# Performance work log

Hardware: AMD Instinct MI355X
Metric: run time of the kernel (lower is better)

The kernel has to match this reference:

```python
import jax, jax.numpy as jnp
import numpy as np

N, E, G = 50000, 800000, 512
F_IN, ED, NUM_CLASSES = 128, 3, 10
H1, C1, C2 = 4, 32, 64


def _add_self_loops(src, dst, eattr, n):
    # PyG add_self_loops with fill_value='mean': loop attr = mean of incoming edge attrs
    cnt = jax.ops.segment_sum(jnp.ones_like(dst, dtype=eattr.dtype), dst, num_segments=n)
    loop = jax.ops.segment_sum(eattr, dst, num_segments=n) / jnp.maximum(cnt, 1.0)[:, None]
    ar = jnp.arange(n)
    return (jnp.concatenate([src, ar]), jnp.concatenate([dst, ar]),
            jnp.concatenate([eattr, loop], axis=0))


def _gatv2(x, src, dst, eattr, Wl, bl, Wr, br, We, att, bias, heads, out_ch, concat, n):
    xl = (x @ Wl.T + bl).reshape(n, heads, out_ch)   # source transform (lin_l)
    xr = (x @ Wr.T + br).reshape(n, heads, out_ch)   # target transform (lin_r)
    ee = (eattr @ We.T).reshape(-1, heads, out_ch)   # edge transform (lin_edge, no bias)
    m = jax.nn.leaky_relu(xl[src] + xr[dst] + ee, 0.2)  # [E', H, C]
    score = jnp.einsum('ehc,hc->eh', m, att)
    # segment softmax over incoming edges of each target node
    smax = jax.ops.segment_max(score, dst, num_segments=n)
    ex = jnp.exp(score - smax[dst])
    denom = jax.ops.segment_sum(ex, dst, num_segments=n)
    alpha = ex / denom[dst]
    out = jax.ops.segment_sum(alpha[:, :, None] * xl[src], dst, num_segments=n)
    out = out.reshape(n, heads * out_ch) if concat else out.mean(axis=1)
    return out + bias


def setup_inputs() -> dict:
    key = jax.random.key(0)
    ks = jax.random.split(key, 24)
    s = 0.1
    return {
        'x': jax.random.normal(ks[0], (N, F_IN), jnp.float32),
        'edge_index': jax.random.randint(ks[1], (2, E), 0, N),
        'edge_attr': jax.random.normal(ks[2], (E, ED), jnp.float32),
        'batch': jnp.sort(jax.random.randint(ks[3], (N,), 0, G)),
        'u': jax.random.normal(ks[4], (G, 1), jnp.float32),
        'Wl1': jax.random.normal(ks[5], (H1 * C1, F_IN), jnp.float32) * s,
        'bl1': jnp.zeros((H1 * C1,), jnp.float32),
        'Wr1': jax.random.normal(ks[6], (H1 * C1, F_IN), jnp.float32) * s,
        'br1': jnp.zeros((H1 * C1,), jnp.float32),
        'We1': jax.random.normal(ks[7], (H1 * C1, ED), jnp.float32) * s,
        'att1': jax.random.normal(ks[8], (H1, C1), jnp.float32) * s,
        'b1': jnp.zeros((H1 * C1,), jnp.float32),
        'Wl2': jax.random.normal(ks[9], (C2, H1 * C1), jnp.float32) * s,
        'bl2': jnp.zeros((C2,), jnp.float32),
        'Wr2': jax.random.normal(ks[10], (C2, H1 * C1), jnp.float32) * s,
        'br2': jnp.zeros((C2,), jnp.float32),
        'We2': jax.random.normal(ks[11], (C2, ED), jnp.float32) * s,
        'att2': jax.random.normal(ks[12], (1, C2), jnp.float32) * s,
        'b2': jnp.zeros((C2,), jnp.float32),
        'W_lin1': jax.random.normal(ks[13], (32, 65), jnp.float32) * s,
        'b_lin1': jnp.zeros((32,), jnp.float32),
        'W_head': jax.random.normal(ks[14], (NUM_CLASSES, 32), jnp.float32) * s,
        'b_head': jnp.zeros((NUM_CLASSES,), jnp.float32),
    }


def reference(x, edge_index, edge_attr, batch, u,
              Wl1, bl1, Wr1, br1, We1, att1, b1,
              Wl2, bl2, Wr2, br2, We2, att2, b2,
              W_lin1, b_lin1, W_head, b_head):
    n = x.shape[0]
    src, dst, ea = _add_self_loops(edge_index[0], edge_index[1], edge_attr, n)
    h = jax.nn.elu(_gatv2(x, src, dst, ea, Wl1, bl1, Wr1, br1, We1, att1, b1, H1, C1, True, n))
    h = jax.nn.elu(_gatv2(h, src, dst, ea, Wl2, bl2, Wr2, br2, We2, att2, b2, 1, C2, False, n))
    cnt = jax.ops.segment_sum(jnp.ones((n,), h.dtype), batch, num_segments=G)
    pooled = jax.ops.segment_sum(h, batch, num_segments=G) / jnp.maximum(cnt, 1.0)[:, None]
    z = jax.nn.relu(jnp.concatenate([pooled, u], axis=1) @ W_lin1.T + b_lin1)
    return z @ W_head.T + b_head
```

## Files before the change

### kernel.cpp

```cpp
#include <hip/hip_runtime.h>
#include <hip/hip_fp16.h>
#include <math.h>


union H2U { __half2 h; unsigned u; };
typedef _Float16 hv2_t __attribute__((ext_vector_type(2)));
typedef unsigned uv4_t __attribute__((ext_vector_type(4)));
typedef _Float16 f16x8 __attribute__((ext_vector_type(8)));
typedef float f32x4 __attribute__((ext_vector_type(4)));

__device__ __forceinline__ __half2 hmax2(__half2 a, __half2 b) {
  union { __half2 h; hv2_t v; } x, y, r;
  x.h = a; y.h = b;
  r.v = __builtin_elementwise_max(x.v, y.v);
  return r.h;
}

#if __has_builtin(__builtin_amdgcn_fdot2)
__device__ __forceinline__ float dot2f(__half2 a, __half2 b, float c) {
  union { __half2 h; hv2_t v; } x, y;
  x.h = a; y.h = b;
  return __builtin_amdgcn_fdot2(x.v, y.v, c, false);
}
#else
__device__ __forceinline__ float dot2f(__half2 a, __half2 b, float c) {
  float2 af = __half22float2(a), bf = __half22float2(b);
  return fmaf(af.x, bf.x, fmaf(af.y, bf.y, c));
}
#endif

#if __has_builtin(__builtin_amdgcn_exp2f)
__device__ __forceinline__ float fexp2(float x) { return __builtin_amdgcn_exp2f(x); }
#else
__device__ __forceinline__ float fexp2(float x) { return exp2f(x); }
#endif

#if __has_builtin(__builtin_amdgcn_update_dpp)
template <int CTRL>
__device__ __forceinline__ float dpp_add(float v) {
  int r = __builtin_amdgcn_update_dpp(0, __builtin_bit_cast(int, v),
                                      CTRL, 0xf, 0xf, true);
  return v + __builtin_bit_cast(float, r);
}
__device__ __forceinline__ float row_sum16(float v) {
  v = dpp_add<0x121>(v);
  v = dpp_add<0x122>(v);
  v = dpp_add<0x124>(v);
  v = dpp_add<0x128>(v);
  return v;
}
__device__ __forceinline__ float row_sum8(float v) {
  v = dpp_add<0xB1>(v);
  v = dpp_add<0x4E>(v);
#if __has_builtin(__builtin_amdgcn_ds_swizzle)
  int sw = __builtin_amdgcn_ds_swizzle(__builtin_bit_cast(int, v), 0x101F);
  return v + __builtin_bit_cast(float, sw);
#else
  return v + __shfl_xor(v, 4);
#endif
}
#else
__device__ __forceinline__ float row_sum16(float v) {
  v += __shfl_xor(v, 1);
  v += __shfl_xor(v, 2);
  v += __shfl_xor(v, 4);
  v += __shfl_xor(v, 8);
  return v;
}
__device__ __forceinline__ float row_sum8(float v) {
  v += __shfl_xor(v, 1);
  v += __shfl_xor(v, 2);
  v += __shfl_xor(v, 4);
  return v;
}
#endif

__device__ __forceinline__ float lowf(unsigned u) {
  H2U t; t.u = u;
  return __half2float(__low2half(t.h));
}

__device__ __forceinline__ float eluf(float x) {
  return x > 0.f ? x : __expf(x) - 1.0f;
}

#define LOG2E 1.44269504088896f

__global__ void hist_k(const int* __restrict__ dst, int* __restrict__ deg,
                       int* __restrict__ rank, int E) {
  int e = blockIdx.x * 256 + threadIdx.x;
  if (e < E) rank[e] = atomicAdd(&deg[dst[e]], 1);
}

__global__ void blocksum_k(const int* __restrict__ deg, int* __restrict__ bsum, int N) {
  __shared__ int s[256];
  int i = blockIdx.x * 256 + threadIdx.x;
  s[threadIdx.x] = (i < N) ? deg[i] : 0;
  __syncthreads();
  for (int off = 128; off; off >>= 1) {
    if (threadIdx.x < off) s[threadIdx.x] += s[threadIdx.x + off];
    __syncthreads();
  }
  if (threadIdx.x == 0) bsum[blockIdx.x] = s[0];
}

__global__ void writeptr_k(const int* __restrict__ deg, const int* __restrict__ bsum,
                           int* __restrict__ rowptr, int N, int E) {
  __shared__ int s[256];
  __shared__ int bs[256];
  int t = threadIdx.x;
  int i = blockIdx.x * 256 + t;
  bs[t] = (t < (int)blockIdx.x) ? bsum[t] : 0;
  s[t] = (i < N) ? deg[i] : 0;
  __syncthreads();
  for (int off = 128; off; off >>= 1) {
    if (t < off) bs[t] += bs[t + off];
    __syncthreads();
  }
  int base = bs[0];
  __syncthreads();
  for (int off = 1; off < 256; off <<= 1) {
    int v = (t >= off) ? s[t - off] : 0;
    __syncthreads();
    if (t >= off) s[t] += v;
    __syncthreads();
  }
  int excl = base + ((t == 0) ? 0 : s[t - 1]) + i;
  if (i < N) rowptr[i] = excl;
  if (i == N - 1) rowptr[N] = E + N;
}

__global__ void fill_k(const int* __restrict__ src, const int* __restrict__ dst,
                       const float* __restrict__ eattr, const int* __restrict__ rowptr,
                       const int* __restrict__ rank, uint4* __restrict__ erec, int E) {
  int e = blockIdx.x * 256 + threadIdx.x;
  if (e >= E) return;
  int pos = rowptr[dst[e]] + rank[e];
  H2U a0, a1, a2;
  float e0 = eattr[e * 3 + 0], e1 = eattr[e * 3 + 1], e2 = eattr[e * 3 + 2];
  a0.h = __floats2half2_rn(e0, e0);
  a1.h = __floats2half2_rn(e1, e1);
  a2.h = __floats2half2_rn(e2, e2);
  uv4_t v = {(unsigned)src[e], a0.u, a1.u, a2.u};
  __builtin_nontemporal_store(v, (uv4_t*)&erec[pos]);
}

__global__ void loopattr_k(const int* __restrict__ rowptr, uint4* __restrict__ erec, int N) {
  int lane = threadIdx.x & 63;
  int n = (int)((blockIdx.x * 256 + threadIdx.x) >> 6);
  if (n >= N) return;
  int beg = rowptr[n], endr = rowptr[n + 1] - 1;
  float f0 = 0.f, f1 = 0.f, f2 = 0.f;
  for (int i = beg + lane; i < endr; i += 64) {
    uint4 r = erec[i];
    f0 += lowf(r.y);
    f1 += lowf(r.z);
    f2 += lowf(r.w);
  }
#pragma unroll
  for (int off = 1; off < 64; off <<= 1) {
    f0 += __shfl_xor(f0, off);
    f1 += __shfl_xor(f1, off);
    f2 += __shfl_xor(f2, off);
  }
  if (lane == 0) {
    float inv = 1.0f / fmaxf((float)(endr - beg), 1.0f);
    H2U a0, a1, a2;
    a0.h = __floats2half2_rn(f0 * inv, f0 * inv);
    a1.h = __floats2half2_rn(f1 * inv, f1 * inv);
    a2.h = __floats2half2_rn(f2 * inv, f2 * inv);
    erec[endr] = make_uint4((unsigned)n, a0.u, a1.u, a2.u);
  }
}

__global__ void cvt_f32_f16_k(const float* __restrict__ src, __half* __restrict__ dst,
                              int n8) {
  int i = blockIdx.x * 256 + threadIdx.x;
  if (i >= n8) return;
  const float4* s = (const float4*)(src + (size_t)i * 8);
  float4 v0 = s[0], v1 = s[1];
  H2U h0, h1, h2, h3;
  h0.h = __floats2half2_rn(v0.x, v0.y);
  h1.h = __floats2half2_rn(v0.z, v0.w);
  h2.h = __floats2half2_rn(v1.x, v1.y);
  h3.h = __floats2half2_rn(v1.z, v1.w);
  uv4_t o = {h0.u, h1.u, h2.u, h3.u};
  *(uv4_t*)(dst + (size_t)i * 8) = o;
}

__global__ void cvt_w_all_k(const float* __restrict__ Wl1, const float* __restrict__ Wr1,
                            const float* __restrict__ Wl2, const float* __restrict__ Wr2,
                            __half* __restrict__ wh1, __half* __restrict__ wh2) {
  int i = blockIdx.x * 256 + threadIdx.x;
  if (i >= 6144) return;
  const float* s;
  __half* d;
  int off;
  if (i < 2048)      { s = Wl1; d = wh1;         off = i; }
  else if (i < 4096) { s = Wr1; d = wh1 + 16384; off = i - 2048; }
  else if (i < 5120) { s = Wl2; d = wh2;         off = i - 4096; }
  else               { s = Wr2; d = wh2 + 8192;  off = i - 5120; }
  const float4* sp = (const float4*)(s + (size_t)off * 8);
  float4 v0 = sp[0], v1 = sp[1];
  H2U h0, h1, h2, h3;
  h0.h = __floats2half2_rn(v0.x, v0.y);
  h1.h = __floats2half2_rn(v0.z, v0.w);
  h2.h = __floats2half2_rn(v1.x, v1.y);
  h3.h = __floats2half2_rn(v1.z, v1.w);
  uv4_t o = {h0.u, h1.u, h2.u, h3.u};
  *(uv4_t*)(d + (size_t)off * 8) = o;
}

template <int J>
__global__ __launch_bounds__(256) void mfma_linear2_k(
    const __half* __restrict__ Xh, const __half* __restrict__ Wh,
    const float* __restrict__ b1v, const float* __restrict__ b2v,
    __half* __restrict__ out1, __half* __restrict__ out2, int N) {
  constexpr int CG = (2 * J) / 64;
  int lane = threadIdx.x & 63;
  int wid = __builtin_amdgcn_readfirstlane(
      (int)((blockIdx.x * 256 + threadIdx.x) >> 6));
  int rt = wid / CG;
  int cg = wid - rt * CG;
  int r0 = rt * 32;
  if (r0 >= N) return;

  int koff = (lane >> 4) * 8;
  int row0 = r0 + (lane & 15);
  int row1 = row0 + 16;
  int cr0 = min(row0, N - 1), cr1 = min(row1, N - 1);

  const __half* xp0 = Xh + (size_t)cr0 * 128 + koff;
  const __half* xp1 = Xh + (size_t)cr1 * 128 + koff;
  f16x8 a0[4], a1[4];
#pragma unroll
  for (int ks = 0; ks < 4; ++ks) {
    a0[ks] = *(const f16x8*)(xp0 + ks * 32);
    a1[ks] = *(const f16x8*)(xp1 + ks * 32);
  }

  bool isT1 = (cg * 64) < J;
  const float* bt = isT1 ? b1v : b2v;
  __half* op = isT1 ? out1 : out2;
  int cbase = cg * 64 - (isT1 ? 0 : J);
  int cl = cbase + (lane & 15);
  int rA = r0 + ((lane >> 4) << 2);

#pragma unroll
  for (int ct = 0; ct < 4; ++ct) {
    int col = cg * 64 + ct * 16 + (lane & 15);
    const __half* wp = Wh + (size_t)col * 128 + koff;
    f16x8 b0 = *(const f16x8*)(wp);
    f16x8 b1_ = *(const f16x8*)(wp + 32);
    f16x8 b2_ = *(const f16x8*)(wp + 64);
    f16x8 b3_ = *(const f16x8*)(wp + 96);
    f32x4 acc0 = {0.f, 0.f, 0.f, 0.f};
    f32x4 acc1 = {0.f, 0.f, 0.f, 0.f};
    acc0 = __builtin_amdgcn_mfma_f32_16x16x32_f16(a0[0], b0, acc0, 0, 0, 0);
    acc1 = __builtin_amdgcn_mfma_f32_16x16x32_f16(a1[0], b0, acc1, 0, 0, 0);
    acc0 = __builtin_amdgcn_mfma_f32_16x16x32_f16(a0[1], b1_, acc0, 0, 0, 0);
    acc1 = __builtin_amdgcn_mfma_f32_16x16x32_f16(a1[1], b1_, acc1, 0, 0, 0);
    acc0 = __builtin_amdgcn_mfma_f32_16x16x32_f16(a0[2], b2_, acc0, 0, 0, 0);
    acc1 = __builtin_amdgcn_mfma_f32_16x16x32_f16(a1[2], b2_, acc1, 0, 0, 0);
    acc0 = __builtin_amdgcn_mfma_f32_16x16x32_f16(a0[3], b3_, acc0, 0, 0, 0);
    acc1 = __builtin_amdgcn_mfma_f32_16x16x32_f16(a1[3], b3_, acc1, 0, 0, 0);

    int cc = cl + ct * 16;
    float bb = bt[cc];
#pragma unroll
    for (int q = 0; q < 4; ++q) {
      int r = rA + q;
      if (r < N) op[(size_t)r * J + cc] = __float2half(acc0[q] + bb);
      int r2 = r + 16;
      if (r2 < N) op[(size_t)r2 * J + cc] = __float2half(acc1[q] + bb);
    }
  }
}

__global__ __launch_bounds__(128) void gat1_fused_k(
    const int* __restrict__ rowptr, const uint4* __restrict__ erec,
    const __half* __restrict__ xlh, const __half* __restrict__ xrh,
    const float* __restrict__ We, const float* __restrict__ att,
    const float* __restrict__ bias, __half* __restrict__ out, int N) {
  int lane = threadIdx.x & 63;
  int sub = lane & 31, grp = lane >> 5;
  int wave0 = __builtin_amdgcn_readfirstlane(
      (int)((blockIdx.x * blockDim.x + threadIdx.x) >> 6));
  int nwaves = (gridDim.x * blockDim.x) >> 6;
  int c4 = sub * 4;

  __half2 w0A = __floats2half2_rn(We[(c4 + 0) * 3 + 0], We[(c4 + 1) * 3 + 0]);
  __half2 w0B = __floats2half2_rn(We[(c4 + 2) * 3 + 0], We[(c4 + 3) * 3 + 0]);
  __half2 w1A = __floats2half2_rn(We[(c4 + 0) * 3 + 1], We[(c4 + 1) * 3 + 1]);
  __half2 w1B = __floats2half2_rn(We[(c4 + 2) * 3 + 1], We[(c4 + 3) * 3 + 1]);
  __half2 w2A = __floats2half2_rn(We[(c4 + 0) * 3 + 2], We[(c4 + 1) * 3 + 2]);
  __half2 w2B = __floats2half2_rn(We[(c4 + 2) * 3 + 2], We[(c4 + 3) * 3 + 2]);
  __half2 attA = __floats2half2_rn(att[c4 + 0] * LOG2E, att[c4 + 1] * LOG2E);
  __half2 attB = __floats2half2_rn(att[c4 + 2] * LOG2E, att[c4 + 3] * LOG2E);
  __half2 k02 = __floats2half2_rn(0.2f, 0.2f);
  float4 bvv = make_float4(bias[c4], bias[c4 + 1], bias[c4 + 2], bias[c4 + 3]);

  for (int n = wave0; n < N; n += nwaves) {
    uint2 xu = *(const uint2*)&xrh[(size_t)n * 128 + c4];
    H2U xrA, xrB;
    xrA.u = xu.x; xrB.u = xu.y;
    int beg = rowptr[n], end = rowptr[n + 1];
    int cnt = end - beg;
    float a0 = 0.f, a1 = 0.f, a2 = 0.f, a3 = 0.f, den = 0.f;

    auto edge2 = [&](const uint4& rec, uint2 gu, bool valid) {
      H2U e0, e1, e2, gA, gB;
      e0.u = rec.y; e1.u = rec.z; e2.u = rec.w;
      gA.u = gu.x; gB.u = gu.y;
      __half2 tA = __hfma2(e2.h, w2A, xrA.h);
      tA = __hfma2(e1.h, w1A, tA);
      tA = __hfma2(e0.h, w0A, tA);
      __half2 mA = __hadd2(gA.h, tA);
      mA = hmax2(mA, __hmul2(mA, k02));
      __half2 tB = __hfma2(e2.h, w2B, xrB.h);
      tB = __hfma2(e1.h, w1B, tB);
      tB = __hfma2(e0.h, w0B, tB);
      __half2 mB = __hadd2(gB.h, tB);
      mB = hmax2(mB, __hmul2(mB, k02));
      float v = dot2f(mB, attB, dot2f(mA, attA, 0.f));
      v = row_sum8(v);
      float ex = valid ? fexp2(v) : 0.f;
      float2 fA = __half22float2(gA.h), fB = __half22float2(gB.h);
      den += ex;
      a0 = fmaf(ex, fA.x, a0);
      a1 = fmaf(ex, fA.y, a1);
      a2 = fmaf(ex, fB.x, a2);
      a3 = fmaf(ex, fB.y, a3);
    };

    int nch = cnt >> 3;
    for (int ch = 0; ch < nch; ++ch) {
      int b = beg + ch * 8 + grp;
      uint4 rec[4];
      uint2 gu[4];
#pragma unroll
      for (int j = 0; j < 4; ++j) rec[j] = erec[b + 2 * j];
#pragma unroll
      for (int j = 0; j < 4; ++j)
        gu[j] = *(const uint2*)(xlh + (size_t)rec[j].x * 128 + c4);
#pragma unroll
      for (int j = 0; j < 4; ++j) edge2(rec[j], gu[j], true);
    }
    for (int gi = beg + nch * 8; gi < end; gi += 2) {
      int idx = gi + grp;
      bool valid = idx < end;
      uint4 rec = erec[valid ? idx : (end - 1)];
      uint2 gu = *(const uint2*)(xlh + (size_t)rec.x * 128 + c4);
      edge2(rec, gu, valid);
    }

    a0 += __shfl_xor(a0, 32);
    a1 += __shfl_xor(a1, 32);
    a2 += __shfl_xor(a2, 32);
    a3 += __shfl_xor(a3, 32);
    den += __shfl_xor(den, 32);

    if (grp == 0) {
      float o0 = eluf(a0 / den + bvv.x);
      float o1 = eluf(a1 / den + bvv.y);
      float o2 = eluf(a2 / den + bvv.z);
      float o3 = eluf(a3 / den + bvv.w);
      H2U p0, p1;
      p0.h = __floats2half2_rn(o0, o1);
      p1.h = __floats2half2_rn(o2, o3);
      *(uint2*)&out[(size_t)n * 128 + c4] = make_uint2(p0.u, p1.u);
    }
  }
}

__global__ __launch_bounds__(128) void gat2_fused_k(
    const int* __restrict__ rowptr, const uint4* __restrict__ erec,
    const __half* __restrict__ xlh, const __half* __restrict__ xrh,
    const float* __restrict__ We, const float* __restrict__ att,
    const float* __restrict__ bias, float* __restrict__ out, int N) {
  int lane = threadIdx.x & 63;
  int s16 = lane & 15, qr = lane >> 4;
  int wave0 = __builtin_amdgcn_readfirstlane(
      (int)((blockIdx.x * blockDim.x + threadIdx.x) >> 6));
  int nwaves = (gridDim.x * blockDim.x) >> 6;
  int c4 = s16 * 4;

  __half2 w0A = __floats2half2_rn(We[(c4 + 0) * 3 + 0], We[(c4 + 1) * 3 + 0]);
  __half2 w0B = __floats2half2_rn(We[(c4 + 2) * 3 + 0], We[(c4 + 3) * 3 + 0]);
  __half2 w1A = __floats2half2_rn(We[(c4 + 0) * 3 + 1], We[(c4 + 1) * 3 + 1]);
  __half2 w1B = __floats2half2_rn(We[(c4 + 2) * 3 + 1], We[(c4 + 3) * 3 + 1]);
  __half2 w2A = __floats2half2_rn(We[(c4 + 0) * 3 + 2], We[(c4 + 1) * 3 + 2]);
  __half2 w2B = __floats2half2_rn(We[(c4 + 2) * 3 + 2], We[(c4 + 3) * 3 + 2]);
  __half2 attA = __floats2half2_rn(att[c4 + 0] * LOG2E, att[c4 + 1] * LOG2E);
  __half2 attB = __floats2half2_rn(att[c4 + 2] * LOG2E, att[c4 + 3] * LOG2E);
  __half2 k02 = __floats2half2_rn(0.2f, 0.2f);
  float4 bvv = make_float4(bias[c4], bias[c4 + 1], bias[c4 + 2], bias[c4 + 3]);

  for (int n = wave0; n < N; n += nwaves) {
    uint2 xu = *(const uint2*)&xrh[(size_t)n * 64 + c4];
    H2U xrA, xrB;
    xrA.u = xu.x; xrB.u = xu.y;
    int beg = rowptr[n], end = rowptr[n + 1];
    int cnt = end - beg;
    float a0 = 0.f, a1 = 0.f, a2 = 0.f, a3 = 0.f, den = 0.f;

    auto edge4 = [&](const uint4& rec, uint2 gu, bool valid) {
      H2U e0, e1, e2, gA, gB;
      e0.u = rec.y; e1.u = rec.z; e2.u = rec.w;
      gA.u = gu.x; gB.u = gu.y;
      __half2 tA = __hfma2(e2.h, w2A, xrA.h);
      tA = __hfma2(e1.h, w1A, tA);
      tA = __hfma2(e0.h, w0A, tA);
      __half2 mA = __hadd2(gA.h, tA);
      mA = hmax2(mA, __hmul2(mA, k02));
      __half2 tB = __hfma2(e2.h, w2B, xrB.h);
      tB = __hfma2(e1.h, w1B, tB);
      tB = __hfma2(e0.h, w0B, tB);
      __half2 mB = __hadd2(gB.h, tB);
      mB = hmax2(mB, __hmul2(mB, k02));
      float v = dot2f(mB, attB, dot2f(mA, attA, 0.f));
      v = row_sum16(v);
      float ex = valid ? fexp2(v) : 0.f;
      float2 fA = __half22float2(gA.h), fB = __half22float2(gB.h);
      den += ex;
      a0 = fmaf(ex, fA.x, a0);
      a1 = fmaf(ex, fA.y, a1);
      a2 = fmaf(ex, fB.x, a2);
      a3 = fmaf(ex, fB.y, a3);
    };

    int nch = cnt >> 3;
    for (int ch = 0; ch < nch; ++ch) {
      int b = beg + ch * 8 + qr;
      uint4 rec[2];
      uint2 gu[2];
#pragma unroll
      for (int j = 0; j < 2; ++j) rec[j] = erec[b + 4 * j];
#pragma unroll
      for (int j = 0; j < 2; ++j)
        gu[j] = *(const uint2*)(xlh + (size_t)rec[j].x * 64 + c4);
#pragma unroll
      for (int j = 0; j < 2; ++j) edge4(rec[j], gu[j], true);
    }
    for (int gi = beg + nch * 8; gi < end; gi += 4) {
      int idx = gi + qr;
      bool valid = idx < end;
      uint4 rec = erec[valid ? idx : (end - 1)];
      uint2 gu = *(const uint2*)(xlh + (size_t)rec.x * 64 + c4);
      edge4(rec, gu, valid);
    }

    a0 += __shfl_xor(a0, 16); a0 += __shfl_xor(a0, 32);
    a1 += __shfl_xor(a1, 16); a1 += __shfl_xor(a1, 32);
    a2 += __shfl_xor(a2, 16); a2 += __shfl_xor(a2, 32);
    a3 += __shfl_xor(a3, 16); a3 += __shfl_xor(a3, 32);
    den += __shfl_xor(den, 16); den += __shfl_xor(den, 32);

    if (lane < 16) {
      float4 o;
      o.x = eluf(a0 / den + bvv.x);
      o.y = eluf(a1 / den + bvv.y);
      o.z = eluf(a2 / den + bvv.z);
      o.w = eluf(a3 / den + bvv.w);
      *(float4*)&out[(size_t)n * 64 + c4] = o;
    }
  }
}

__global__ void final_mlp_k(const float* __restrict__ h2, const int* __restrict__ batch,
                            int N, const float* __restrict__ u,
                            const float* __restrict__ W1, const float* __restrict__ b1,
                            const float* __restrict__ Wh, const float* __restrict__ bh,
                            float* __restrict__ out) {
  __shared__ float comb[4][64];
  __shared__ float feat[65];
  __shared__ float z[32];
  int g = blockIdx.x;
  int t = threadIdx.x;
  int c = t & 63, q = t >> 6;
  int lo, hi;
  {
    int l = 0, h = N;
    while (l < h) { int m = (l + h) >> 1; if (batch[m] < g) l = m + 1; else h = m; }
    lo = l;
    h = N;
    while (l < h) { int m = (l + h) >> 1; if (batch[m] < g + 1) l = m + 1; else h = m; }
    hi = l;
  }
  float a = 0.f;
  for (int nn = lo + q; nn < hi; nn += 4) a += h2[(size_t)nn * 64 + c];
  comb[q][c] = a;
  __syncthreads();
  if (t < 64) {
    float s = comb[0][t] + comb[1][t] + comb[2][t] + comb[3][t];
    float inv = 1.0f / fmaxf((float)(hi - lo), 1.0f);
    feat[t] = s * inv;
    if (t == 0) feat[64] = u[g];
  }
  __syncthreads();
  if (t < 32) {
    float s = b1[t];
    for (int k = 0; k < 65; ++k) s += feat[k] * W1[t * 65 + k];
    z[t] = fmaxf(s, 0.0f);
  }
  __syncthreads();
  if (t < 10) {
    float s = bh[t];
    for (int k = 0; k < 32; ++k) s += z[k] * Wh[t * 32 + k];
    out[g * 10 + t] = s;
  }
}

extern "C" void kernel_launch(void* const* d_in, const int* in_sizes, int n_in,
                              void* d_out, int out_size, void* d_ws, size_t ws_size,
                              hipStream_t stream) {
  const float* x      = (const float*)d_in[0];
  const int*   eidx   = (const int*)d_in[1];
  const float* eattr  = (const float*)d_in[2];
  const int*   batch  = (const int*)d_in[3];
  const float* u      = (const float*)d_in[4];
  const float* Wl1    = (const float*)d_in[5];
  const float* bl1    = (const float*)d_in[6];
  const float* Wr1    = (const float*)d_in[7];
  const float* br1    = (const float*)d_in[8];
  const float* We1    = (const float*)d_in[9];
  const float* att1   = (const float*)d_in[10];
  const float* b1     = (const float*)d_in[11];
  const float* Wl2    = (const float*)d_in[12];
  const float* bl2    = (const float*)d_in[13];
  const float* Wr2    = (const float*)d_in[14];
  const float* br2    = (const float*)d_in[15];
  const float* We2    = (const float*)d_in[16];
  const float* att2   = (const float*)d_in[17];
  const float* b2     = (const float*)d_in[18];
  const float* W_lin1 = (const float*)d_in[19];
  const float* b_lin1 = (const float*)d_in[20];
  const float* W_head = (const float*)d_in[21];
  const float* b_head = (const float*)d_in[22];

  const int N = in_sizes[0] / 128;
  const int E = in_sizes[1] / 2;
  const int G = in_sizes[4];
  const int* srcp = eidx;
  const int* dstp = eidx + E;

  __half* bufh = (__half*)d_ws;
  __half* bufr = bufh + (size_t)N * 128;
  float* buf3 = (float*)(bufr + (size_t)N * 128);
  __half* g1h = (__half*)buf3;
  float* h2f = (float*)(g1h + (size_t)N * 128);
  uint4* erec = (uint4*)(buf3 + (size_t)N * 128);
  __half* xh  = (__half*)erec;
  int* rank   = (int*)(erec + ((size_t)E + N));
  int* deg    = rank + E;
  int* rowptr = deg + N;
  int* bsum   = rowptr + N + 1;
  uintptr_t wtop = ((uintptr_t)(bsum + 256) + 15) & ~(uintptr_t)15;
  __half* wh1 = (__half*)wtop;
  __half* wh2 = wh1 + 32768;

  const int nb = (N + 255) / 256;
  const int gat_blocks = (N + 1) / 2;
  const int rt = (N + 31) / 32;

  cvt_w_all_k<<<24, 256, 0, stream>>>(Wl1, Wr1, Wl2, Wr2, wh1, wh2);
  cvt_f32_f16_k<<<(N * 16 + 255) / 256, 256, 0, stream>>>(x, xh, N * 16);
  mfma_linear2_k<128><<<rt, 256, 0, stream>>>(xh, wh1, bl1, br1, bufh, bufr, N);

  (void)hipMemsetAsync(deg, 0, sizeof(int) * (size_t)N, stream);
  hist_k<<<(E + 255) / 256, 256, 0, stream>>>(dstp, deg, rank, E);
  blocksum_k<<<nb, 256, 0, stream>>>(deg, bsum, N);
  writeptr_k<<<nb, 256, 0, stream>>>(deg, bsum, rowptr, N, E);
  fill_k<<<(E + 255) / 256, 256, 0, stream>>>(srcp, dstp, eattr, rowptr, rank, erec, E);
  loopattr_k<<<(N * 64 + 255) / 256, 256, 0, stream>>>(rowptr, erec, N);

  gat1_fused_k<<<gat_blocks, 128, 0, stream>>>(rowptr, erec, bufh, bufr,
                                               We1, att1, b1, g1h, N);

  mfma_linear2_k<64><<<(rt * 2 + 3) / 4, 256, 0, stream>>>(g1h, wh2, bl2, br2,
                                                           bufh, bufr, N);
  gat2_fused_k<<<gat_blocks, 128, 0, stream>>>(rowptr, erec, bufh, bufr,
                                               We2, att2, b2, h2f, N);

  final_mlp_k<<<G, 256, 0, stream>>>(h2f, batch, N, u, W_lin1, b_lin1, W_head, b_head,
                                     (float*)d_out);
}
```

Measured before the change: 338.1 us.

## Process one edge per wave in GAT layer 1 with 2 channels per lane

Restructures the layer-1 fused attention kernel so the whole 64-lane wave processes one edge at a time, with each lane owning two channels, instead of two half-waves each taking an edge with four channels per lane. The source index is made wave-uniform via readfirstlane, which enables scalar addressing, and edges are batched in chunks of 8, then 4, 2 and 1 for the tail. This removes the cross-half shuffle reduction and the masked invalid-edge work, but it doubles the number of serial edge iterations per node and uses a 16-lane reduction per head instead of an 8-lane one.

```diff
diff --git a/kernel.cpp b/kernel.cpp
--- a/kernel.cpp
+++ b/kernel.cpp
@@ -49,28 +49,12 @@
   v = dpp_add<0x128>(v);
   return v;
 }
-__device__ __forceinline__ float row_sum8(float v) {
-  v = dpp_add<0xB1>(v);
-  v = dpp_add<0x4E>(v);
-#if __has_builtin(__builtin_amdgcn_ds_swizzle)
-  int sw = __builtin_amdgcn_ds_swizzle(__builtin_bit_cast(int, v), 0x101F);
-  return v + __builtin_bit_cast(float, sw);
-#else
-  return v + __shfl_xor(v, 4);
-#endif
-}
 #else
 __device__ __forceinline__ float row_sum16(float v) {
   v += __shfl_xor(v, 1);
   v += __shfl_xor(v, 2);
   v += __shfl_xor(v, 4);
   v += __shfl_xor(v, 8);
-  return v;
-}
-__device__ __forceinline__ float row_sum8(float v) {
-  v += __shfl_xor(v, 1);
-  v += __shfl_xor(v, 2);
-  v += __shfl_xor(v, 4);
   return v;
 }
 #endif
@@ -282,94 +266,99 @@
     const __half* __restrict__ xlh, const __half* __restrict__ xrh,
     const float* __restrict__ We, const float* __restrict__ att,
     const float* __restrict__ bias, __half* __restrict__ out, int N) {
+  constexpr int CH = 8;
   int lane = threadIdx.x & 63;
-  int sub = lane & 31, grp = lane >> 5;
   int wave0 = __builtin_amdgcn_readfirstlane(
       (int)((blockIdx.x * blockDim.x + threadIdx.x) >> 6));
   int nwaves = (gridDim.x * blockDim.x) >> 6;
-  int c4 = sub * 4;
-
-  __half2 w0A = __floats2half2_rn(We[(c4 + 0) * 3 + 0], We[(c4 + 1) * 3 + 0]);
-  __half2 w0B = __floats2half2_rn(We[(c4 + 2) * 3 + 0], We[(c4 + 3) * 3 + 0]);
-  __half2 w1A = __floats2half2_rn(We[(c4 + 0) * 3 + 1], We[(c4 + 1) * 3 + 1]);
-  __half2 w1B = __floats2half2_rn(We[(c4 + 2) * 3 + 1], We[(c4 + 3) * 3 + 1]);
-  __half2 w2A = __floats2half2_rn(We[(c4 + 0) * 3 + 2], We[(c4 + 1) * 3 + 2]);
-  __half2 w2B = __floats2half2_rn(We[(c4 + 2) * 3 + 2], We[(c4 + 3) * 3 + 2]);
-  __half2 attA = __floats2half2_rn(att[c4 + 0] * LOG2E, att[c4 + 1] * LOG2E);
-  __half2 attB = __floats2half2_rn(att[c4 + 2] * LOG2E, att[c4 + 3] * LOG2E);
+  const __half2* xl2p = (const __half2*)xlh;
+  const __half2* xr2p = (const __half2*)xrh;
+  __half2* outp = (__half2*)out;
+  int c0 = 2 * lane;
+  __half2 w0p = __floats2half2_rn(We[c0 * 3 + 0], We[c0 * 3 + 3]);
+  __half2 w1p = __floats2half2_rn(We[c0 * 3 + 1], We[c0 * 3 + 4]);
+  __half2 w2p = __floats2half2_rn(We[c0 * 3 + 2], We[c0 * 3 + 5]);
+  __half2 attp = __floats2half2_rn(att[c0] * LOG2E, att[c0 + 1] * LOG2E);
   __half2 k02 = __floats2half2_rn(0.2f, 0.2f);
-  float4 bvv = make_float4(bias[c4], bias[c4 + 1], bias[c4 + 2], bias[c4 + 3]);
+  float2 bv = make_float2(bias[c0], bias[c0 + 1]);
 
   for (int n = wave0; n < N; n += nwaves) {
-    uint2 xu = *(const uint2*)&xrh[(size_t)n * 128 + c4];
-    H2U xrA, xrB;
-    xrA.u = xu.x; xrB.u = xu.y;
+    __half2 xrp = xr2p[(size_t)n * 64 + lane];
     int beg = rowptr[n], end = rowptr[n + 1];
     int cnt = end - beg;
-    float a0 = 0.f, a1 = 0.f, a2 = 0.f, a3 = 0.f, den = 0.f;
-
-    auto edge2 = [&](const uint4& rec, uint2 gu, bool valid) {
-      H2U e0, e1, e2, gA, gB;
+
+    float acc0 = 0.f, acc1 = 0.f, den = 0.f;
+
+    auto edge1 = [&](const uint4& rec, __half2 rf) {
+      H2U e0, e1, e2;
       e0.u = rec.y; e1.u = rec.z; e2.u = rec.w;
-      gA.u = gu.x; gB.u = gu.y;
-      __half2 tA = __hfma2(e2.h, w2A, xrA.h);
-      tA = __hfma2(e1.h, w1A, tA);
-      tA = __hfma2(e0.h, w0A, tA);
-      __half2 mA = __hadd2(gA.h, tA);
-      mA = hmax2(mA, __hmul2(mA, k02));
-      __half2 tB = __hfma2(e2.h, w2B, xrB.h);
-      tB = __hfma2(e1.h, w1B, tB);
-      tB = __hfma2(e0.h, w0B, tB);
-      __half2 mB = __hadd2(gB.h, tB);
-      mB = hmax2(mB, __hmul2(mB, k02));
-      float v = dot2f(mB, attB, dot2f(mA, attA, 0.f));
-      v = row_sum8(v);
-      float ex = valid ? fexp2(v) : 0.f;
-      float2 fA = __half22float2(gA.h), fB = __half22float2(gB.h);
+      __half2 m = __hadd2(rf, xrp);
+      m = __hfma2(e0.h, w0p, m);
+      m = __hfma2(e1.h, w1p, m);
+      m = __hfma2(e2.h, w2p, m);
+      m = hmax2(m, __hmul2(m, k02));
+      float v = row_sum16(dot2f(m, attp, 0.f));
+      float ex = fexp2(v);
+      float2 rfF = __half22float2(rf);
       den += ex;
-      a0 = fmaf(ex, fA.x, a0);
-      a1 = fmaf(ex, fA.y, a1);
-      a2 = fmaf(ex, fB.x, a2);
-      a3 = fmaf(ex, fB.y, a3);
+      acc0 = fmaf(ex, rfF.x, acc0);
+      acc1 = fmaf(ex, rfF.y, acc1);
     };
 
-    int nch = cnt >> 3;
-    for (int ch = 0; ch < nch; ++ch) {
-      int b = beg + ch * 8 + grp;
-      uint4 rec[4];
-      uint2 gu[4];
-#pragma unroll
-      for (int j = 0; j < 4; ++j) rec[j] = erec[b + 2 * j];
-#pragma unroll
-      for (int j = 0; j < 4; ++j)
-        gu[j] = *(const uint2*)(xlh + (size_t)rec[j].x * 128 + c4);
-#pragma unroll
-      for (int j = 0; j < 4; ++j) edge2(rec[j], gu[j], true);
-    }
-    for (int gi = beg + nch * 8; gi < end; gi += 2) {
-      int idx = gi + grp;
-      bool valid = idx < end;
-      uint4 rec = erec[valid ? idx : (end - 1)];
-      uint2 gu = *(const uint2*)(xlh + (size_t)rec.x * 128 + c4);
-      edge2(rec, gu, valid);
-    }
-
-    a0 += __shfl_xor(a0, 32);
-    a1 += __shfl_xor(a1, 32);
-    a2 += __shfl_xor(a2, 32);
-    a3 += __shfl_xor(a3, 32);
-    den += __shfl_xor(den, 32);
-
-    if (grp == 0) {
-      float o0 = eluf(a0 / den + bvv.x);
-      float o1 = eluf(a1 / den + bvv.y);
-      float o2 = eluf(a2 / den + bvv.z);
-      float o3 = eluf(a3 / den + bvv.w);
-      H2U p0, p1;
-      p0.h = __floats2half2_rn(o0, o1);
-      p1.h = __floats2half2_rn(o2, o3);
-      *(uint2*)&out[(size_t)n * 128 + c4] = make_uint2(p0.u, p1.u);
-    }
+    int nfull = cnt / CH;
+    for (int ch = 0; ch < nfull; ++ch) {
+      int b = beg + ch * CH;
+      uint4 recs[CH];
+#pragma unroll
+      for (int j = 0; j < CH; ++j) recs[j] = erec[b + j];
+      __half2 r_[CH];
+#pragma unroll
+      for (int j = 0; j < CH; ++j) {
+        int s = __builtin_amdgcn_readfirstlane((int)recs[j].x);
+        r_[j] = xl2p[(size_t)s * 64 + lane];
+      }
+#pragma unroll
+      for (int j = 0; j < CH; ++j) edge1(recs[j], r_[j]);
+    }
+    int gi = beg + nfull * CH;
+    if (gi + 4 <= end) {
+      uint4 recs[4];
+#pragma unroll
+      for (int j = 0; j < 4; ++j) recs[j] = erec[gi + j];
+      __half2 r_[4];
+#pragma unroll
+      for (int j = 0; j < 4; ++j) {
+        int s = __builtin_amdgcn_readfirstlane((int)recs[j].x);
+        r_[j] = xl2p[(size_t)s * 64 + lane];
+      }
+#pragma unroll
+      for (int j = 0; j < 4; ++j) edge1(recs[j], r_[j]);
+      gi += 4;
+    }
+    for (; gi + 2 <= end; gi += 2) {
+      uint4 recA = erec[gi];
+      uint4 recB = erec[gi + 1];
+      int sA = __builtin_amdgcn_readfirstlane((int)recA.x);
+      int sB = __builtin_amdgcn_readfirstlane((int)recB.x);
+      __half2 rfA = xl2p[(size_t)sA * 64 + lane];
+      __half2 rfB = xl2p[(size_t)sB * 64 + lane];
+      edge1(recA, rfA);
+      edge1(recB, rfB);
+    }
+    if (gi < end) {
+      uint4 rec = erec[gi];
+      int s = __builtin_amdgcn_readfirstlane((int)rec.x);
+      __half2 rf = xl2p[(size_t)s * 64 + lane];
+      edge1(rec, rf);
+    }
+
+    float o0 = acc0 / den + bv.x;
+    float o1 = acc1 / den + bv.y;
+    o0 = o0 > 0.f ? o0 : __expf(o0) - 1.0f;
+    o1 = o1 > 0.f ? o1 : __expf(o1) - 1.0f;
+    H2U o;
+    o.h = __floats2half2_rn(o0, o1);
+    outp[(size_t)n * 64 + lane] = o.h;
   }
 }
 
```

Result: no change. 334.6 us (-1.0%).
